# Optimization experiments

Hardware: AMD Instinct MI355X
Metric: run time of the kernel (lower is better)

## Reference

```python
import jax, jax.numpy as jnp
import numpy as np

NUM_ENTITIES = 100000
NUM_RELATIONS = 1000
ENTITY_DIM = 256
RELATION_DIM = 256
BATCH = 8192


def setup_inputs() -> dict:
    key = jax.random.key(0)
    k1, k2, k3, k4, k5, k6 = jax.random.split(key, 6)
    bound_e = 6.0 / np.sqrt(ENTITY_DIM)
    bound_r = 6.0 / np.sqrt(RELATION_DIM)
    entity_embed = jax.random.uniform(k1, (NUM_ENTITIES, ENTITY_DIM), jnp.float32, -bound_e, bound_e)
    relation_embed = jax.random.uniform(k2, (NUM_RELATIONS, RELATION_DIM), jnp.float32, -bound_r, bound_r)
    # proj matrices initialized near identity (TransR convention) plus small noise
    eye = jnp.broadcast_to(jnp.eye(RELATION_DIM, ENTITY_DIM, dtype=jnp.float32), (NUM_RELATIONS, RELATION_DIM, ENTITY_DIM))
    proj = (eye + 0.01 * jax.random.normal(k3, (NUM_RELATIONS, RELATION_DIM, ENTITY_DIM), jnp.float32)).reshape(NUM_RELATIONS, RELATION_DIM * ENTITY_DIM)
    h = jax.random.randint(k4, (BATCH,), 0, NUM_ENTITIES)
    r = jax.random.randint(k5, (BATCH,), 0, NUM_RELATIONS)
    t = jax.random.randint(k6, (BATCH,), 0, NUM_ENTITIES)
    return {"h": h, "r": r, "t": t, "entity_embed": entity_embed,
            "relation_embed": relation_embed, "proj": proj}


def reference(h, r, t, entity_embed, relation_embed, proj) -> jnp.ndarray:
    # gather embeddings
    h_emb = entity_embed[h]                      # [B, ed]
    t_emb = entity_embed[t]                      # [B, ed]
    r_emb = relation_embed[r]                    # [B, rd]
    M = proj[r].reshape(-1, RELATION_DIM, ENTITY_DIM)  # [B, rd, ed]
    # batched matvec: project head/tail into relation space
    h_r = jnp.einsum('bre,be->br', M, h_emb)     # [B, rd]
    t_r = jnp.einsum('bre,be->br', M, t_emb)     # [B, rd]
    diff = h_r + r_emb - t_r
    return -jnp.sqrt(jnp.sum(diff * diff, axis=-1))  # [B]
```

## Files before the change

### kernel.cpp

```cpp
#include <hip/hip_runtime.h>
#include <math.h>


#define ED   256
#define TR64 64
#define NT   4
#define CAP  64

typedef __attribute__((ext_vector_type(8))) short bf16x8;
typedef __attribute__((ext_vector_type(4))) float f32x4;

__device__ __forceinline__ unsigned int bfbits_rne(float x) {
    unsigned int u = __builtin_bit_cast(unsigned int, x);
    return (u + 0x7fffu + ((u >> 16) & 1u)) >> 16;
}
__device__ __forceinline__ unsigned int pack2(float x, float y) {
    return bfbits_rne(x) | (bfbits_rne(y) << 16);
}

__global__ void transr_prep_kernel(const int* __restrict__ h, const int* __restrict__ t,
                                   const float* __restrict__ ent, int B,
                                   uint4* __restrict__ Dbf)
{
    int i = blockIdx.x * 256 + threadIdx.x;
    if (i < B * 32) {
        int b = i >> 5, c = i & 31;
        const float4* hv = (const float4*)ent + (size_t)h[b] * 64 + c * 2;
        const float4* tv = (const float4*)ent + (size_t)t[b] * 64 + c * 2;
        float4 a0 = hv[0], a1 = hv[1], b0 = tv[0], b1 = tv[1];
        uint4 o;
        o.x = pack2(a0.x - b0.x, a0.y - b0.y);
        o.y = pack2(a0.z - b0.z, a0.w - b0.w);
        o.z = pack2(a1.x - b1.x, a1.y - b1.y);
        o.w = pack2(a1.z - b1.z, a1.w - b1.w);
        Dbf[i] = o;
    }
}

__global__ __launch_bounds__(256, 4)
void transr_mfma_kernel(const int* __restrict__ r, const float* __restrict__ rel,
                        const float* __restrict__ proj, const uint4* __restrict__ Dbf,
                        float* __restrict__ part, int B)
{
    __shared__ __align__(16) unsigned short Mt[TR64 * ED];
    __shared__ int items_s[CAP];
    __shared__ int s_n;

    const int relid = blockIdx.x;
    const int tile  = blockIdx.y;
    const int tid   = threadIdx.x;

    int4 rv[8];
    #pragma unroll
    for (int j = 0; j < 8; ++j) {
        int i0 = tid * 4 + j * 1024;
        if (i0 < B) rv[j] = *(const int4*)(r + i0);
        else        rv[j] = make_int4(-1, -1, -1, -1);
    }

    const float4* Mg4 = (const float4*)(proj + (size_t)relid * ED * ED
                                             + (size_t)tile * TR64 * ED);
    float4 ra[8], rb[8];
    #pragma unroll
    for (int it = 0; it < 8; ++it) {
        ra[it] = Mg4[2 * (tid + 256 * it)];
        rb[it] = Mg4[2 * (tid + 256 * it) + 1];
    }

    if (tid == 0) s_n = 0;
    __syncthreads();

    #pragma unroll
    for (int j = 0; j < 8; ++j) {
        int i0 = tid * 4 + j * 1024;
        if (i0 < B) {
            int4 v = rv[j];
            if (v.x == relid) { int p = atomicAdd(&s_n, 1); if (p < CAP) items_s[p] = i0;     }
            if (v.y == relid) { int p = atomicAdd(&s_n, 1); if (p < CAP) items_s[p] = i0 + 1; }
            if (v.z == relid) { int p = atomicAdd(&s_n, 1); if (p < CAP) items_s[p] = i0 + 2; }
            if (v.w == relid) { int p = atomicAdd(&s_n, 1); if (p < CAP) items_s[p] = i0 + 3; }
        }
    }
    __syncthreads();

    const int n = min(s_n, CAP);
    if (n == 0) return;

    #pragma unroll
    for (int it = 0; it < 8; ++it) {
        int f  = tid + 256 * it;
        int rr = f >> 5, c = f & 31;
        uint4 o;
        o.x = pack2(ra[it].x, ra[it].y); o.y = pack2(ra[it].z, ra[it].w);
        o.z = pack2(rb[it].x, rb[it].y); o.w = pack2(rb[it].z, rb[it].w);
        *(uint4*)&Mt[rr * ED + ((c ^ (rr & 7)) << 3)] = o;
    }

    const int l    = tid & 63;
    const int w    = tid >> 6;
    const int li   = l & 15;
    const int lk   = l >> 4;
    const int arow = w * 16 + li;
    const int aswz = arow & 7;

    f32x4 rbv = *(const f32x4*)(rel + (size_t)relid * ED + tile * TR64 + w * 16 + lk * 4);

    __syncthreads();

    for (int c0 = 0; c0 < n; c0 += 16) {
        const int bslot = min(c0 + li, n - 1);
        const uint4* bbase = Dbf + (size_t)items_s[bslot] * 32;

        f32x4 acc = {0.f, 0.f, 0.f, 0.f};
        #pragma unroll
        for (int kk = 0; kk < 8; ++kk) {
            bf16x8 av = *(const bf16x8*)&Mt[arow * ED + (((kk * 4 + lk) ^ aswz) << 3)];
            bf16x8 bv = __builtin_bit_cast(bf16x8, bbase[kk * 4 + lk]);
            acc = __builtin_amdgcn_mfma_f32_16x16x32_bf16(av, bv, acc, 0, 0, 0);
        }

        float s = 0.f;
        #pragma unroll
        for (int j = 0; j < 4; ++j) {
            float v = acc[j] + rbv[j];
            s = fmaf(v, v, s);
        }
        s += __shfl_xor(s, 16);
        s += __shfl_xor(s, 32);
        if (lk == 0 && c0 + li < n)
            part[(size_t)items_s[c0 + li] * 16 + tile * 4 + w] = s;
    }
}

__global__ void transr_finalize_kernel(const float* __restrict__ part,
                                       float* __restrict__ out, int B)
{
    int i = blockIdx.x * 256 + threadIdx.x;
    if (i < B) {
        const float4* p = (const float4*)(part + (size_t)i * 16);
        float4 a = p[0], b = p[1], c = p[2], d = p[3];
        float s = a.x + a.y + a.z + a.w;
        s += b.x + b.y + b.z + b.w;
        s += c.x + c.y + c.z + c.w;
        s += d.x + d.y + d.z + d.w;
        out[i] = -sqrtf(s);
    }
}

#define FNCH 16
#define FCAP 2048
__global__ __launch_bounds__(256, 1)
void transr_score_kernel(const int* __restrict__ h, const int* __restrict__ r,
                         const int* __restrict__ t, const float* __restrict__ ent,
                         const float* __restrict__ rel, const float* __restrict__ proj,
                         float* __restrict__ out, int B)
{
    __shared__ int   items[FCAP];
    __shared__ int   s_n;
    __shared__ __align__(16) float D[FNCH][ED];
    __shared__ __align__(16) float Mt2[32][ED];
    __shared__ float remb[ED];
    __shared__ float sacc2[FNCH];

    const int relid = blockIdx.x;
    const int tid   = threadIdx.x;
    if (tid == 0) s_n = 0;
    __syncthreads();

    for (int i0 = tid * 4; i0 < B; i0 += 256 * 4) {
        int4 rv = *(const int4*)(r + i0);
        if (rv.x == relid) { int p = atomicAdd(&s_n, 1); if (p < FCAP) items[p] = i0;     }
        if (rv.y == relid) { int p = atomicAdd(&s_n, 1); if (p < FCAP) items[p] = i0 + 1; }
        if (rv.z == relid) { int p = atomicAdd(&s_n, 1); if (p < FCAP) items[p] = i0 + 2; }
        if (rv.w == relid) { int p = atomicAdd(&s_n, 1); if (p < FCAP) items[p] = i0 + 3; }
    }
    remb[tid] = rel[(size_t)relid * ED + tid];
    __syncthreads();

    int n = s_n < FCAP ? s_n : FCAP;
    if (n == 0) return;

    const float* Mg = proj + (size_t)relid * (ED * ED);
    const int rt = tid & 31, g = tid >> 5, sw = rt & 7;

    for (int c0 = 0; c0 < n; c0 += FNCH) {
        const int nc = min(FNCH, n - c0);
        {
            const int j  = tid >> 4;
            const int e4 = tid & 15;
            if (j < nc) {
                const int b = items[c0 + j];
                const float4* hv = (const float4*)(ent + (size_t)h[b] * ED);
                const float4* tv = (const float4*)(ent + (size_t)t[b] * ED);
                #pragma unroll
                for (int k = 0; k < 4; ++k) {
                    float4 a = hv[e4 + 16 * k];
                    float4 c = tv[e4 + 16 * k];
                    float4 d4; d4.x = a.x - c.x; d4.y = a.y - c.y;
                               d4.z = a.z - c.z; d4.w = a.w - c.w;
                    *(float4*)&D[j][4 * (e4 + 16 * k)] = d4;
                }
            } else {
                float4 z; z.x = z.y = z.z = z.w = 0.f;
                #pragma unroll
                for (int k = 0; k < 4; ++k) *(float4*)&D[j][4 * (e4 + 16 * k)] = z;
            }
        }
        __syncthreads();

        float sq0 = 0.f, sq1 = 0.f;
        for (int tile = 0; tile < 8; ++tile) {
            const float4* Mg4 = (const float4*)(Mg + (size_t)tile * 32 * ED);
            #pragma unroll
            for (int k = 0; k < 8; ++k) {
                int f = tid + 256 * k;
                int rr = f >> 6, e4 = f & 63;
                *(float4*)&Mt2[rr][4 * (e4 ^ (rr & 7))] = Mg4[f];
            }
            __syncthreads();

            float acc0 = 0.f, acc1 = 0.f;
            #pragma unroll 8
            for (int e4 = 0; e4 < 64; ++e4) {
                float4 m  = *(const float4*)&Mt2[rt][4 * (e4 ^ sw)];
                float4 d0 = *(const float4*)&D[g][4 * e4];
                float4 d1 = *(const float4*)&D[g + 8][4 * e4];
                acc0 = fmaf(m.x, d0.x, acc0); acc0 = fmaf(m.y, d0.y, acc0);
                acc0 = fmaf(m.z, d0.z, acc0); acc0 = fmaf(m.w, d0.w, acc0);
                acc1 = fmaf(m.x, d1.x, acc1); acc1 = fmaf(m.y, d1.y, acc1);
                acc1 = fmaf(m.z, d1.z, acc1); acc1 = fmaf(m.w, d1.w, acc1);
            }
            const float rb = remb[tile * 32 + rt];
            float s0 = acc0 + rb; s0 *= s0;
            float s1 = acc1 + rb; s1 *= s1;
            #pragma unroll
            for (int off = 16; off >= 1; off >>= 1) {
                s0 += __shfl_xor(s0, off, 32);
                s1 += __shfl_xor(s1, off, 32);
            }
            sq0 += s0; sq1 += s1;
            __syncthreads();
        }
        if (rt == 0) { sacc2[g] = sq0; sacc2[g + 8] = sq1; }
        __syncthreads();
        if (tid < nc) out[items[c0 + tid]] = -sqrtf(sacc2[tid]);
        __syncthreads();
    }
}

extern "C" void kernel_launch(void* const* d_in, const int* in_sizes, int n_in,
                              void* d_out, int out_size, void* d_ws, size_t ws_size,
                              hipStream_t stream)
{
    const int*   h    = (const int*)d_in[0];
    const int*   r    = (const int*)d_in[1];
    const int*   t    = (const int*)d_in[2];
    const float* ent  = (const float*)d_in[3];
    const float* rel  = (const float*)d_in[4];
    const float* proj = (const float*)d_in[5];
    float*       out  = (float*)d_out;

    const int B  = in_sizes[0];
    const int NR = in_sizes[5] / (ED * ED);

    size_t o_part = 0;
    size_t o_D    = (o_part + (size_t)B * 16 * 4 + 255) & ~(size_t)255;
    size_t need   = o_D + (size_t)B * ED * 2;

    if (ws_size >= need && B <= 8192 && (B & 3) == 0) {
        float* part = (float*)((char*)d_ws + o_part);
        uint4* Dbf  = (uint4*)((char*)d_ws + o_D);

        transr_prep_kernel<<<(B * 32 + 255) / 256, 256, 0, stream>>>(h, t, ent, B, Dbf);
        transr_mfma_kernel<<<dim3(NR, NT), 256, 0, stream>>>(r, rel, proj, Dbf, part, B);
        transr_finalize_kernel<<<(B + 255) / 256, 256, 0, stream>>>(part, out, B);
    } else {
        transr_score_kernel<<<NR, 256, 0, stream>>>(h, r, t, ent, rel, proj, out, B);
    }
}
```

Measured before the change: 55.93 us.

## Fuse head-tail difference gather into MFMA kernel and drop prep pass

```diff
diff --git a/kernel.cpp b/kernel.cpp
--- a/kernel.cpp
+++ b/kernel.cpp
@@ -18,29 +18,11 @@
     return bfbits_rne(x) | (bfbits_rne(y) << 16);
 }
 
-__global__ void transr_prep_kernel(const int* __restrict__ h, const int* __restrict__ t,
-                                   const float* __restrict__ ent, int B,
-                                   uint4* __restrict__ Dbf)
-{
-    int i = blockIdx.x * 256 + threadIdx.x;
-    if (i < B * 32) {
-        int b = i >> 5, c = i & 31;
-        const float4* hv = (const float4*)ent + (size_t)h[b] * 64 + c * 2;
-        const float4* tv = (const float4*)ent + (size_t)t[b] * 64 + c * 2;
-        float4 a0 = hv[0], a1 = hv[1], b0 = tv[0], b1 = tv[1];
-        uint4 o;
-        o.x = pack2(a0.x - b0.x, a0.y - b0.y);
-        o.y = pack2(a0.z - b0.z, a0.w - b0.w);
-        o.z = pack2(a1.x - b1.x, a1.y - b1.y);
-        o.w = pack2(a1.z - b1.z, a1.w - b1.w);
-        Dbf[i] = o;
-    }
-}
-
 __global__ __launch_bounds__(256, 4)
-void transr_mfma_kernel(const int* __restrict__ r, const float* __restrict__ rel,
-                        const float* __restrict__ proj, const uint4* __restrict__ Dbf,
-                        float* __restrict__ part, int B)
+void transr_fused_kernel(const int* __restrict__ h, const int* __restrict__ r,
+                         const int* __restrict__ t, const float* __restrict__ ent,
+                         const float* __restrict__ rel, const float* __restrict__ proj,
+                         float* __restrict__ part, int B)
 {
     __shared__ __align__(16) unsigned short Mt[TR64 * ED];
     __shared__ int items_s[CAP];
@@ -49,6 +31,8 @@
     const int relid = blockIdx.x;
     const int tile  = blockIdx.y;
     const int tid   = threadIdx.x;
+    const int l     = tid & 63;
+    const int w     = tid >> 6;
 
     int4 rv[8];
     #pragma unroll
@@ -58,13 +42,14 @@
         else        rv[j] = make_int4(-1, -1, -1, -1);
     }
 
-    const float4* Mg4 = (const float4*)(proj + (size_t)relid * ED * ED
-                                             + (size_t)tile * TR64 * ED);
+    const float4* Mg4w = (const float4*)(proj + (size_t)relid * ED * ED
+                                              + ((size_t)tile * TR64 + w * 16) * ED);
     float4 ra[8], rb[8];
     #pragma unroll
-    for (int it = 0; it < 8; ++it) {
-        ra[it] = Mg4[2 * (tid + 256 * it)];
-        rb[it] = Mg4[2 * (tid + 256 * it) + 1];
+    for (int jj = 0; jj < 8; ++jj) {
+        int idx = jj * 128 + 2 * l;
+        ra[jj] = Mg4w[idx];
+        rb[jj] = Mg4w[idx + 1];
     }
 
     if (tid == 0) s_n = 0;
@@ -87,17 +72,16 @@
     if (n == 0) return;
 
     #pragma unroll
-    for (int it = 0; it < 8; ++it) {
-        int f  = tid + 256 * it;
-        int rr = f >> 5, c = f & 31;
+    for (int jj = 0; jj < 8; ++jj) {
+        int idx   = jj * 128 + 2 * l;
+        int row   = w * 16 + (idx >> 6);
+        int cc    = (idx & 63) >> 1;
         uint4 o;
-        o.x = pack2(ra[it].x, ra[it].y); o.y = pack2(ra[it].z, ra[it].w);
-        o.z = pack2(rb[it].x, rb[it].y); o.w = pack2(rb[it].z, rb[it].w);
-        *(uint4*)&Mt[rr * ED + ((c ^ (rr & 7)) << 3)] = o;
-    }
-
-    const int l    = tid & 63;
-    const int w    = tid >> 6;
+        o.x = pack2(ra[jj].x, ra[jj].y); o.y = pack2(ra[jj].z, ra[jj].w);
+        o.z = pack2(rb[jj].x, rb[jj].y); o.w = pack2(rb[jj].z, rb[jj].w);
+        *(uint4*)&Mt[row * ED + ((cc ^ (row & 7)) << 3)] = o;
+    }
+
     const int li   = l & 15;
     const int lk   = l >> 4;
     const int arow = w * 16 + li;
@@ -105,18 +89,30 @@
 
     f32x4 rbv = *(const f32x4*)(rel + (size_t)relid * ED + tile * TR64 + w * 16 + lk * 4);
 
-    __syncthreads();
-
     for (int c0 = 0; c0 < n; c0 += 16) {
-        const int bslot = min(c0 + li, n - 1);
-        const uint4* bbase = Dbf + (size_t)items_s[bslot] * 32;
+        const int item = items_s[min(c0 + li, n - 1)];
+        const f32x4* hp = (const f32x4*)(ent + (size_t)h[item] * ED);
+        const f32x4* tp = (const f32x4*)(ent + (size_t)t[item] * ED);
+
+        bf16x8 bfr[8];
+        #pragma unroll
+        for (int kk = 0; kk < 8; ++kk) {
+            int c2 = (kk * 4 + lk) * 2;
+            f32x4 h0 = hp[c2], h1 = hp[c2 + 1];
+            f32x4 t0 = tp[c2], t1 = tp[c2 + 1];
+            uint4 o;
+            o.x = pack2(h0[0] - t0[0], h0[1] - t0[1]);
+            o.y = pack2(h0[2] - t0[2], h0[3] - t0[3]);
+            o.z = pack2(h1[0] - t1[0], h1[1] - t1[1]);
+            o.w = pack2(h1[2] - t1[2], h1[3] - t1[3]);
+            bfr[kk] = __builtin_bit_cast(bf16x8, o);
+        }
 
         f32x4 acc = {0.f, 0.f, 0.f, 0.f};
         #pragma unroll
         for (int kk = 0; kk < 8; ++kk) {
             bf16x8 av = *(const bf16x8*)&Mt[arow * ED + (((kk * 4 + lk) ^ aswz) << 3)];
-            bf16x8 bv = __builtin_bit_cast(bf16x8, bbase[kk * 4 + lk]);
-            acc = __builtin_amdgcn_mfma_f32_16x16x32_bf16(av, bv, acc, 0, 0, 0);
+            acc = __builtin_amdgcn_mfma_f32_16x16x32_bf16(av, bfr[kk], acc, 0, 0, 0);
         }
 
         float s = 0.f;
@@ -128,7 +124,7 @@
         s += __shfl_xor(s, 16);
         s += __shfl_xor(s, 32);
         if (lk == 0 && c0 + li < n)
-            part[(size_t)items_s[c0 + li] * 16 + tile * 4 + w] = s;
+            part[(size_t)item * 16 + tile * 4 + w] = s;
     }
 }
 
@@ -263,16 +259,12 @@
     const int B  = in_sizes[0];
     const int NR = in_sizes[5] / (ED * ED);
 
-    size_t o_part = 0;
-    size_t o_D    = (o_part + (size_t)B * 16 * 4 + 255) & ~(size_t)255;
-    size_t need   = o_D + (size_t)B * ED * 2;
+    size_t need = (size_t)B * 16 * 4;
 
     if (ws_size >= need && B <= 8192 && (B & 3) == 0) {
-        float* part = (float*)((char*)d_ws + o_part);
-        uint4* Dbf  = (uint4*)((char*)d_ws + o_D);
-
-        transr_prep_kernel<<<(B * 32 + 255) / 256, 256, 0, stream>>>(h, t, ent, B, Dbf);
-        transr_mfma_kernel<<<dim3(NR, NT), 256, 0, stream>>>(r, rel, proj, Dbf, part, B);
+        float* part = (float*)d_ws;
+        transr_fused_kernel<<<dim3(NR, NT), 256, 0, stream>>>(h, r, t, ent, rel,
+                                                              proj, part, B);
         transr_finalize_kernel<<<(B + 255) / 256, 256, 0, stream>>>(part, out, B);
     } else {
         transr_score_kernel<<<NR, 256, 0, stream>>>(h, r, t, ent, rel, proj, out, B);
```

After: 94.54 us. 1.69x slower.
